# Kernel optimization log

Measured on AMD Instinct MI355X. Metric: run time of the kernel, lower is better.

## Reference

```python
import jax, jax.numpy as jnp
import numpy as np

B, S, D = 4, 4096, 2048
DECAY_BIAS_INIT = -4.0
W_SCALE = 0.02


def setup_inputs() -> dict:
    key = jax.random.key(0)
    ks = jax.random.split(key, 6)
    return {
        "x": jax.random.normal(ks[0], (B, S, D), dtype=jnp.float32),
        "W_in": jax.random.normal(ks[1], (D, D), dtype=jnp.float32) * W_SCALE,
        "b_in": jnp.zeros((D,), jnp.float32),
        "W_decay": jax.random.normal(ks[2], (D, D), dtype=jnp.float32) * W_SCALE,
        "b_decay": jnp.zeros((D,), jnp.float32),
        "W_gate": jax.random.normal(ks[3], (D, D), dtype=jnp.float32) * W_SCALE,
        "b_gate": jnp.zeros((D,), jnp.float32),
        "W_out": jax.random.normal(ks[4], (D, D), dtype=jnp.float32) * W_SCALE,
        "b_out": jnp.zeros((D,), jnp.float32),
        "decay_bias": jnp.full((D,), DECAY_BIAS_INIT, jnp.float32),
    }


def reference(x, W_in, b_in, W_decay, b_decay, W_gate, b_gate, W_out, b_out, decay_bias):
    # Projections (weights stored as [in, out]; torch Linear applies x @ W.T, here W is pre-transposed)
    inp = jax.nn.silu(jnp.einsum("bsd,de->bse", x, W_in) + b_in).astype(jnp.float32)
    decay = jax.nn.sigmoid(jnp.einsum("bsd,de->bse", x, W_decay) + b_decay + decay_bias)
    gate = jax.nn.sigmoid(jnp.einsum("bsd,de->bse", x, W_gate) + b_gate)

    # Gated linear recurrence: s_t = d_t * s_{t-1} + (1 - d_t) * i_t
    def step(state, di):
        d, i = di
        state = d * state + (1.0 - d) * i
        return state, state

    init = jnp.zeros((x.shape[0], x.shape[2]), jnp.float32)
    _, states = jax.lax.scan(
        step, init, (jnp.swapaxes(decay, 0, 1), jnp.swapaxes(inp, 0, 1))
    )  # states: [S, B, D]
    y = gate * jnp.swapaxes(states, 0, 1)  # [B, S, D]
    y = y.astype(x.dtype)
    return jnp.einsum("bsd,de->bse", y, W_out) + b_out
```

## Files before the change

### kernel.cpp

```cpp
#include <hip/hip_runtime.h>

typedef unsigned short u16;
typedef __attribute__((ext_vector_type(4))) float f4;
typedef __attribute__((ext_vector_type(8))) short s8v;
typedef __attribute__((ext_vector_type(8))) unsigned short u16x8;
typedef __attribute__((ext_vector_type(4))) unsigned short u16x4;

#define B_   4
#define S_   4096
#define D_   2048
#define M_   (B_ * S_)
#define K_   D_
#define N3_  (3 * D_)
#define CCH  128
#define LCH  32
#define NTK  32
#define SCH  8
#define SCL  16

__device__ __forceinline__ u16 f2bf(float f) {
  unsigned u = __float_as_uint(f);
  u += 0x7FFF + ((u >> 16) & 1);
  return (u16)(u >> 16);
}
__device__ __forceinline__ float bf2f(u16 h) {
  return __uint_as_float(((unsigned)h) << 16);
}
__device__ __forceinline__ float sigm(float z) {
  return 1.0f / (1.0f + __expf(-z));
}

__global__ void k_cvt(const float* __restrict__ src, u16* __restrict__ dst, int n4) {
  for (int i = blockIdx.x * 256 + threadIdx.x; i < n4; i += 2048 * 256) {
    f4 v = *(const f4*)(src + (size_t)i * 4);
    u16x4 o;
    o[0] = f2bf(v[0]); o[1] = f2bf(v[1]); o[2] = f2bf(v[2]); o[3] = f2bf(v[3]);
    *(u16x4*)(dst + (size_t)i * 4) = o;
  }
}

__global__ void k_tcvt4(const float* __restrict__ W_in, const float* __restrict__ W_dec,
                        const float* __restrict__ W_gate, const float* __restrict__ W_out,
                        u16* __restrict__ w3t, u16* __restrict__ wot) {
  __shared__ float tile[32][33];
  const float* src = (blockIdx.z == 0) ? W_in : (blockIdx.z == 1) ? W_dec
                    : (blockIdx.z == 2) ? W_gate : W_out;
  u16* dst = (blockIdx.z < 3) ? (w3t + (size_t)blockIdx.z * 2048 * 2048) : wot;
  int tx = threadIdx.x & 31, ty = threadIdx.x >> 5;
  int c0 = blockIdx.x * 32, r0 = blockIdx.y * 32;
#pragma unroll
  for (int j = 0; j < 32; j += 8)
    tile[ty + j][tx] = src[(size_t)(r0 + ty + j) * 2048 + c0 + tx];
  __syncthreads();
#pragma unroll
  for (int j = 0; j < 32; j += 8)
    dst[(size_t)(c0 + ty + j) * 2048 + r0 + tx] = f2bf(tile[tx][ty + j]);
}

__global__ void __launch_bounds__(512, 2)
k_gemm256(const u16* __restrict__ A, const u16* __restrict__ BT, int N, int mode,
          u16* __restrict__ o_inp, u16* __restrict__ o_dec, u16* __restrict__ o_gate,
          const float* __restrict__ b_in, const float* __restrict__ b_dec,
          const float* __restrict__ b_gate, const float* __restrict__ dbias,
          float* __restrict__ o_f, const float* __restrict__ b_out) {
  extern __shared__ u16 smem[];
  u16* const Asb[2] = { smem,         smem + 16384 };
  u16* const Bsb[2] = { smem + 32768, smem + 49152 };

  const int bid = blockIdx.x;
  const int xcd = bid & 7, j = bid >> 3;
  const int nsb = j >> 6;
  const int rj = j & 63;
  const int mm = rj >> 3, nn = rj & 7;
  const int tile_m = ((xcd << 3) + mm) << 8;
  const int tile_n = ((nsb << 3) + nn) << 8;

  const int tid = threadIdx.x;
  const int wave = tid >> 6, lane = tid & 63;
  const int wm = (wave >> 2) << 7;
  const int wn = (wave & 3) << 6;
  const int l15 = lane & 15, lhi = lane >> 4;
  const int srow = tid >> 3, sslot = tid & 7;

  f4 acc[8][4];
#pragma unroll
  for (int m = 0; m < 8; ++m)
#pragma unroll
    for (int n = 0; n < 4; ++n)
#pragma unroll
      for (int r = 0; r < 4; ++r) acc[m][n][r] = 0.0f;

  s8v afr2[2][2][2];
  s8v bfr[2][4];

  const int swz = l15 & 7;
  const u16* ap[2][2];
  const u16* bp[2][2];
#pragma unroll
  for (int b = 0; b < 2; ++b)
#pragma unroll
    for (int kk = 0; kk < 2; ++kk) {
      const int so = ((((kk << 2) + lhi) ^ swz) << 3);
      ap[b][kk] = Asb[b] + ((wm + l15) << 6) + so;
      bp[b][kk] = Bsb[b] + ((wn + l15) << 6) + so;
    }
  const int gl = srow * K_ + ((sslot ^ (srow & 7)) << 3);

  auto STAGE = [&](const u16* __restrict__ G, int grow0, u16* L, int c, int k0) {
    const u16* src = G + (size_t)(grow0 + (c << 6)) * K_ + k0;
    __builtin_amdgcn_global_load_lds(
        (const __attribute__((address_space(1))) unsigned int*)(src + gl),
        (__attribute__((address_space(3))) unsigned int*)(L + (((c << 6) + (wave << 3)) << 6)),
        16, 0, 0);
  };

#pragma unroll
  for (int c = 0; c < 4; ++c) STAGE(A, tile_m, Asb[0], c, 0);
#pragma unroll
  for (int c = 0; c < 4; ++c) STAGE(BT, tile_n, Bsb[0], c, 0);
#pragma unroll
  for (int c = 0; c < 4; ++c) STAGE(BT, tile_n, Bsb[1], c, 64);
  STAGE(A, tile_m, Asb[1], 0, 64);
  STAGE(A, tile_m, Asb[1], 2, 64);
  asm volatile("s_waitcnt vmcnt(6)" ::: "memory");
  __builtin_amdgcn_s_barrier();

#pragma unroll
  for (int kk = 0; kk < 2; ++kk)
#pragma unroll
    for (int mi = 0; mi < 2; ++mi)
      afr2[0][mi][kk] = *(const s8v*)(ap[0][kk] + (mi << 10));
#pragma unroll
  for (int kk = 0; kk < 2; ++kk)
#pragma unroll
    for (int n = 0; n < 4; ++n)
      bfr[kk][n] = *(const s8v*)(bp[0][kk] + (n << 10));

#pragma unroll 1
  for (int it = 0; it < NTK / 2; ++it) {
    const int t0 = it << 1;
#pragma unroll
    for (int p = 0; p < 8; ++p) {
      const int toff[8] = {1, 2, 2, 2, 2, 3, 3, 3};
      const int sopA[8] = {1, 0, 0, 1, 1, 0, 0, 1};
      const int sc0[8]  = {1, 0, 2, 0, 1, 0, 2, 0};
      const int sc1f[8] = {3, 1, 3, 2, 3, 1, 3, 2};
      const int q = p & 3;

      {
        const int st = (t0 + toff[p]) & (NTK - 1);
        const int k0s = st << 6;
        u16* const Ad = Asb[st & 1];
        u16* const Bd = Bsb[st & 1];
        if (sopA[p]) { STAGE(A, tile_m, Ad, sc0[p], k0s); STAGE(A, tile_m, Ad, sc1f[p], k0s); }
        else         { STAGE(BT, tile_n, Bd, sc0[p], k0s); STAGE(BT, tile_n, Bd, sc1f[p], k0s); }
      }
      if (q == 3) {
        asm volatile("s_waitcnt vmcnt(6)" ::: "memory");
        __builtin_amdgcn_sched_barrier(0);
      }
      __builtin_amdgcn_s_barrier();

      {
        const int pn = p + 1;
        const int qn = pn & 3, bn = (pn >> 2) & 1, as = pn & 1;
#pragma unroll
        for (int kk = 0; kk < 2; ++kk)
#pragma unroll
          for (int mi = 0; mi < 2; ++mi)
            afr2[as][mi][kk] = *(const s8v*)(ap[bn][kk] + (((qn << 1) + mi) << 10));
      }

      __builtin_amdgcn_s_setprio(1);
#pragma unroll
      for (int kk = 0; kk < 2; ++kk)
#pragma unroll
        for (int mi = 0; mi < 2; ++mi)
#pragma unroll
          for (int n = 0; n < 4; ++n)
            acc[q * 2 + mi][n] =
                __builtin_amdgcn_mfma_f32_16x16x32_bf16(afr2[p & 1][mi][kk], bfr[kk][n],
                                                        acc[q * 2 + mi][n], 0, 0, 0);
      __builtin_amdgcn_s_setprio(0);

      if (q == 3) {
        const int bn = ((p + 1) >> 2) & 1;
#pragma unroll
        for (int kk = 0; kk < 2; ++kk)
#pragma unroll
          for (int n = 0; n < 4; ++n)
            bfr[kk][n] = *(const s8v*)(bp[bn][kk] + (n << 10));
      }
    }
  }

  asm volatile("s_waitcnt vmcnt(0)" ::: "memory");
  __builtin_amdgcn_s_barrier();

  if (mode == 0) {
    const int selb = tile_n >> 11;
    const int dbase = tile_n & 2047;
    float bias[4];
#pragma unroll
    for (int n = 0; n < 4; ++n) {
      int d = dbase + wn + (n << 4) + l15;
      bias[n] = (selb == 0) ? b_in[d] : (selb == 1) ? (b_dec[d] + dbias[d]) : b_gate[d];
    }
#pragma unroll
    for (int m = 0; m < 8; ++m)
#pragma unroll
      for (int n = 0; n < 4; ++n)
#pragma unroll
        for (int r = 0; r < 4; ++r) {
          int lrow = wm + (m << 4) + (lhi << 2) + r;
          int lcol = wn + (n << 4) + l15;
          float z = acc[m][n][r] + bias[n];
          float v = (selb == 0) ? z * sigm(z) : sigm(z);
          smem[(lrow << 8) + (((lcol >> 3) ^ (lrow & 7)) << 3) + (lcol & 7)] = f2bf(v);
        }
    __builtin_amdgcn_s_barrier();
    u16* const dst = (selb == 0) ? o_inp : (selb == 1) ? o_dec : o_gate;
    const int rr = tid >> 5, sl = tid & 31;
#pragma unroll
    for (int pass = 0; pass < 16; ++pass) {
      int row = (pass << 4) + rr;
      u16x8 v = *(const u16x8*)(smem + (row << 8) + ((sl ^ (row & 7)) << 3));
      *(u16x8*)(dst + (size_t)(tile_m + row) * D_ + dbase + (sl << 3)) = v;
    }
  } else {
    float* const Tf = (float*)smem;
    f4 bo = *(const f4*)(b_out + tile_n + (lane << 2));
#pragma unroll
    for (int sw = 0; sw < 2; ++sw) {
      if (sw) __builtin_amdgcn_s_barrier();
      if ((wm >> 7) == sw) {
#pragma unroll
        for (int m = 0; m < 8; ++m)
#pragma unroll
          for (int n = 0; n < 4; ++n)
#pragma unroll
            for (int r = 0; r < 4; ++r) {
              int lrow = (m << 4) + (lhi << 2) + r;
              int lcol = wn + (n << 4) + l15;
              Tf[(lrow << 8) + (((lcol >> 2) ^ (lrow & 7)) << 2) + (lcol & 3)] = acc[m][n][r];
            }
      }
      __builtin_amdgcn_s_barrier();
#pragma unroll
      for (int pass = 0; pass < 16; ++pass) {
        int lrow = (pass << 3) + wave;
        f4 v = *(const f4*)(Tf + (lrow << 8) + ((lane ^ (lrow & 7)) << 2));
        v[0] += bo[0]; v[1] += bo[1]; v[2] += bo[2]; v[3] += bo[3];
        *(f4*)(o_f + (size_t)(tile_m + (sw << 7) + lrow) * D_ + tile_n + (lane << 2)) = v;
      }
    }
  }
}

__global__ void k_scan1(const u16* __restrict__ dec, const u16* __restrict__ inp,
                        float* __restrict__ chA, float* __restrict__ chB) {
  int b = blockIdx.x / CCH, c = blockIdx.x % CCH;
  int d0 = threadIdx.x * 8;
  const u16* dp = dec + ((size_t)b * S_ + c * LCH) * D_ + d0;
  const u16* ip = inp + ((size_t)b * S_ + c * LCH) * D_ + d0;
  float Aa[8], st[8];
#pragma unroll
  for (int i = 0; i < 8; ++i) { Aa[i] = 1.0f; st[i] = 0.0f; }
#pragma unroll 4
  for (int j = 0; j < LCH; ++j) {
    u16x8 dv = *(const u16x8*)(dp + (size_t)j * D_);
    u16x8 iv = *(const u16x8*)(ip + (size_t)j * D_);
#pragma unroll
    for (int i = 0; i < 8; ++i) {
      float dd = bf2f(dv[i]), ii = bf2f(iv[i]);
      Aa[i] *= dd;
      st[i] = dd * st[i] + (1.0f - dd) * ii;
    }
  }
  size_t o = ((size_t)b * CCH + c) * D_ + d0;
#pragma unroll
  for (int i = 0; i < 8; ++i) { chA[o + i] = Aa[i]; chB[o + i] = st[i]; }
}

__global__ void k_scan2a(const float* __restrict__ chA, const float* __restrict__ chB,
                         float* __restrict__ sA, float* __restrict__ sB) {
  int gid = blockIdx.x * 256 + threadIdx.x;
  int d = gid & (D_ - 1);
  int s = (gid >> 11) & (SCH - 1);
  int b = gid >> 14;
  float Aa = 1.0f, Bb = 0.0f;
  for (int c = 0; c < SCL; ++c) {
    size_t o = ((size_t)b * CCH + s * SCL + c) * D_ + d;
    float a = chA[o], bb = chB[o];
    Aa *= a;
    Bb = a * Bb + bb;
  }
  size_t so = ((size_t)b * SCH + s) * D_ + d;
  sA[so] = Aa; sB[so] = Bb;
}

__global__ void k_scan2b(const float* __restrict__ sA, const float* __restrict__ sB,
                         float* __restrict__ sI) {
  int gid = blockIdx.x * 256 + threadIdx.x;
  int d = gid & (D_ - 1);
  int b = gid >> 11;
  float st = 0.0f;
  for (int s = 0; s < SCH; ++s) {
    size_t o = ((size_t)b * SCH + s) * D_ + d;
    sI[o] = st;
    st = sA[o] * st + sB[o];
  }
}

__global__ void k_scan2c(const float* __restrict__ chA, const float* __restrict__ chB,
                         const float* __restrict__ sI, float* __restrict__ ini) {
  int gid = blockIdx.x * 256 + threadIdx.x;
  int d = gid & (D_ - 1);
  int s = (gid >> 11) & (SCH - 1);
  int b = gid >> 14;
  float st = sI[((size_t)b * SCH + s) * D_ + d];
  for (int c = 0; c < SCL; ++c) {
    size_t o = ((size_t)b * CCH + s * SCL + c) * D_ + d;
    ini[o] = st;
    st = chA[o] * st + chB[o];
  }
}

__global__ void k_scan3(const u16* __restrict__ dec, const u16* __restrict__ inp,
                        const u16* __restrict__ gat, const float* __restrict__ ini,
                        u16* __restrict__ y) {
  int b = blockIdx.x / CCH, c = blockIdx.x % CCH;
  int d0 = threadIdx.x * 8;
  size_t ib = ((size_t)b * CCH + c) * D_ + d0;
  float st[8];
#pragma unroll
  for (int i = 0; i < 8; ++i) st[i] = ini[ib + i];
  size_t base = ((size_t)b * S_ + c * LCH) * D_ + d0;
#pragma unroll 4
  for (int j = 0; j < LCH; ++j) {
    size_t o = base + (size_t)j * D_;
    u16x8 dv = *(const u16x8*)(dec + o);
    u16x8 iv = *(const u16x8*)(inp + o);
    u16x8 gv = *(const u16x8*)(gat + o);
    u16x8 yv;
#pragma unroll
    for (int i = 0; i < 8; ++i) {
      float dd = bf2f(dv[i]), ii = bf2f(iv[i]);
      st[i] = dd * st[i] + (1.0f - dd) * ii;
      yv[i] = f2bf(bf2f(gv[i]) * st[i]);
    }
    *(u16x8*)(y + o) = yv;
  }
}

extern "C" void kernel_launch(void* const* d_in, const int* in_sizes, int n_in,
                              void* d_out, int out_size, void* d_ws, size_t ws_size,
                              hipStream_t stream) {
  (void)in_sizes; (void)n_in; (void)out_size; (void)ws_size;
  const float* x      = (const float*)d_in[0];
  const float* W_in   = (const float*)d_in[1];
  const float* b_in   = (const float*)d_in[2];
  const float* W_dec  = (const float*)d_in[3];
  const float* b_dec  = (const float*)d_in[4];
  const float* W_gate = (const float*)d_in[5];
  const float* b_gate = (const float*)d_in[6];
  const float* W_out  = (const float*)d_in[7];
  const float* b_out  = (const float*)d_in[8];
  const float* dbias  = (const float*)d_in[9];
  float* out = (float*)d_out;

  char* ws = (char*)d_ws;
  u16*   xb  = (u16*)(ws);
  u16*   w3t = (u16*)(ws + 67108864ull);
  u16*   wot = (u16*)(ws + 92274688ull);
  u16*   inp = (u16*)(ws + 100663296ull);
  u16*   dec = (u16*)(ws + 167772160ull);
  u16*   gat = (u16*)(ws + 234881024ull);
  float* chA = (float*)(ws + 301989888ull);
  float* chB = (float*)(ws + 306184192ull);
  float* ini = (float*)(ws + 310378496ull);
  float* sA  = (float*)(ws + 314572800ull);
  float* sB  = (float*)(ws + 314834944ull);
  float* sI  = (float*)(ws + 315097088ull);
  u16*   y   = xb;

  hipFuncSetAttribute((const void*)k_gemm256,
                      hipFuncAttributeMaxDynamicSharedMemorySize, 131072);

  k_cvt<<<2048, 256, 0, stream>>>(x, xb, 8388608);
  k_tcvt4<<<dim3(64, 64, 4), 256, 0, stream>>>(W_in, W_dec, W_gate, W_out, w3t, wot);

  k_gemm256<<<(M_ / 256) * (N3_ / 256), 512, 131072, stream>>>(
      xb, w3t, N3_, 0, inp, dec, gat, b_in, b_dec, b_gate, dbias, nullptr, nullptr);

  k_scan1<<<B_ * CCH, 256, 0, stream>>>(dec, inp, chA, chB);
  k_scan2a<<<256, 256, 0, stream>>>(chA, chB, sA, sB);
  k_scan2b<<<32, 256, 0, stream>>>(sA, sB, sI);
  k_scan2c<<<256, 256, 0, stream>>>(chA, chB, sI, ini);
  k_scan3<<<B_ * CCH, 256, 0, stream>>>(dec, inp, gat, ini, y);

  k_gemm256<<<(M_ / 256) * (D_ / 256), 512, 131072, stream>>>(
      y, wot, D_, 1, nullptr, nullptr, nullptr, nullptr, nullptr, nullptr, nullptr,
      out, b_out);
}
```

Baseline: 631.8 us.

## Replace 256x256 GEMM tile with 128x256 tile, K=32 steps and higher occupancy

Rewrites the projection/output GEMM kernel to use 128x256 block tiles with K-step 32 instead of 256x256 with K-step 64. LDS use drops from 128KB to 48KB and launch bounds rise to 4 blocks per CU, trading per-block data reuse for more concurrent blocks and twice as many grid tiles. The pipeline schedule, swizzle addressing and epilogues are rewritten to match. Smaller tiles mean more global/L2 traffic per FLOP and more barriers per K-iteration.

```diff
diff --git a/kernel.cpp b/kernel.cpp
--- a/kernel.cpp
+++ b/kernel.cpp
@@ -14,9 +14,9 @@
 #define N3_  (3 * D_)
 #define CCH  128
 #define LCH  32
-#define NTK  32
 #define SCH  8
 #define SCL  16
+#define NKT  64
 
 __device__ __forceinline__ u16 f2bf(float f) {
   unsigned u = __float_as_uint(f);
@@ -57,140 +57,109 @@
     dst[(size_t)(c0 + ty + j) * 2048 + r0 + tx] = f2bf(tile[tx][ty + j]);
 }
 
-__global__ void __launch_bounds__(512, 2)
-k_gemm256(const u16* __restrict__ A, const u16* __restrict__ BT, int N, int mode,
+__global__ void __launch_bounds__(512, 4)
+k_gemm128(const u16* __restrict__ A, const u16* __restrict__ BT, int N, int mode,
           u16* __restrict__ o_inp, u16* __restrict__ o_dec, u16* __restrict__ o_gate,
           const float* __restrict__ b_in, const float* __restrict__ b_dec,
           const float* __restrict__ b_gate, const float* __restrict__ dbias,
           float* __restrict__ o_f, const float* __restrict__ b_out) {
   extern __shared__ u16 smem[];
-  u16* const Asb[2] = { smem,         smem + 16384 };
-  u16* const Bsb[2] = { smem + 32768, smem + 49152 };
+  u16* const As0 = smem;
+  u16* const As1 = smem + 4096;
+  u16* const Bs0 = smem + 8192;
+  u16* const Bs1 = smem + 16384;
 
   const int bid = blockIdx.x;
   const int xcd = bid & 7, j = bid >> 3;
-  const int nsb = j >> 6;
-  const int rj = j & 63;
-  const int mm = rj >> 3, nn = rj & 7;
-  const int tile_m = ((xcd << 3) + mm) << 8;
-  const int tile_n = ((nsb << 3) + nn) << 8;
+  const int tile_m = ((xcd << 4) + (j & 15)) << 7;
+  const int tile_n = (j >> 4) << 8;
 
   const int tid = threadIdx.x;
   const int wave = tid >> 6, lane = tid & 63;
-  const int wm = (wave >> 2) << 7;
+  const int wm = (wave >> 2) << 6;
   const int wn = (wave & 3) << 6;
   const int l15 = lane & 15, lhi = lane >> 4;
-  const int srow = tid >> 3, sslot = tid & 7;
-
-  f4 acc[8][4];
-#pragma unroll
-  for (int m = 0; m < 8; ++m)
+
+  const int slog = (tid & 7) ^ ((tid >> 3) & 7);
+  const int gl = ((((tid >> 3) << 1) + (slog >> 2)) * K_) + ((slog & 3) << 3);
+  const int ldst = (wave << 9);
+
+  const int phys = (((l15 & 1) << 2) + lhi) ^ ((l15 >> 1) & 7);
+  const int rbase = ((l15 >> 1) << 6) + (phys << 3);
+  const u16* const apb[2] = { As0 + (wm << 5) + rbase, As1 + (wm << 5) + rbase };
+  const u16* const bpb[2] = { Bs0 + (wn << 5) + rbase, Bs1 + (wn << 5) + rbase };
+
+  f4 acc[4][4];
+#pragma unroll
+  for (int m = 0; m < 4; ++m)
 #pragma unroll
     for (int n = 0; n < 4; ++n)
 #pragma unroll
       for (int r = 0; r < 4; ++r) acc[m][n][r] = 0.0f;
 
-  s8v afr2[2][2][2];
-  s8v bfr[2][4];
-
-  const int swz = l15 & 7;
-  const u16* ap[2][2];
-  const u16* bp[2][2];
-#pragma unroll
-  for (int b = 0; b < 2; ++b)
-#pragma unroll
-    for (int kk = 0; kk < 2; ++kk) {
-      const int so = ((((kk << 2) + lhi) ^ swz) << 3);
-      ap[b][kk] = Asb[b] + ((wm + l15) << 6) + so;
-      bp[b][kk] = Bsb[b] + ((wn + l15) << 6) + so;
-    }
-  const int gl = srow * K_ + ((sslot ^ (srow & 7)) << 3);
+  s8v afr2[2][2];
+  s8v bfr[4];
 
   auto STAGE = [&](const u16* __restrict__ G, int grow0, u16* L, int c, int k0) {
-    const u16* src = G + (size_t)(grow0 + (c << 6)) * K_ + k0;
+    const u16* src = G + (size_t)(grow0 + (c << 7)) * K_ + k0;
     __builtin_amdgcn_global_load_lds(
         (const __attribute__((address_space(1))) unsigned int*)(src + gl),
-        (__attribute__((address_space(3))) unsigned int*)(L + (((c << 6) + (wave << 3)) << 6)),
+        (__attribute__((address_space(3))) unsigned int*)(L + (c << 12) + ldst),
         16, 0, 0);
   };
 
-#pragma unroll
-  for (int c = 0; c < 4; ++c) STAGE(A, tile_m, Asb[0], c, 0);
-#pragma unroll
-  for (int c = 0; c < 4; ++c) STAGE(BT, tile_n, Bsb[0], c, 0);
-#pragma unroll
-  for (int c = 0; c < 4; ++c) STAGE(BT, tile_n, Bsb[1], c, 64);
-  STAGE(A, tile_m, Asb[1], 0, 64);
-  STAGE(A, tile_m, Asb[1], 2, 64);
-  asm volatile("s_waitcnt vmcnt(6)" ::: "memory");
+  STAGE(A, tile_m, As0, 0, 0);
+  STAGE(BT, tile_n, Bs0, 0, 0); STAGE(BT, tile_n, Bs0, 1, 0);
+  STAGE(A, tile_m, As1, 0, 32);
+  STAGE(BT, tile_n, Bs1, 0, 32); STAGE(BT, tile_n, Bs1, 1, 32);
+  asm volatile("s_waitcnt vmcnt(3)" ::: "memory");
   __builtin_amdgcn_s_barrier();
-
-#pragma unroll
-  for (int kk = 0; kk < 2; ++kk)
-#pragma unroll
-    for (int mi = 0; mi < 2; ++mi)
-      afr2[0][mi][kk] = *(const s8v*)(ap[0][kk] + (mi << 10));
-#pragma unroll
-  for (int kk = 0; kk < 2; ++kk)
-#pragma unroll
-    for (int n = 0; n < 4; ++n)
-      bfr[kk][n] = *(const s8v*)(bp[0][kk] + (n << 10));
+#pragma unroll
+  for (int i = 0; i < 2; ++i) afr2[0][i] = *(const s8v*)(apb[0] + i * 512);
+#pragma unroll
+  for (int nf = 0; nf < 4; ++nf) bfr[nf] = *(const s8v*)(bpb[0] + nf * 512);
 
 #pragma unroll 1
-  for (int it = 0; it < NTK / 2; ++it) {
-    const int t0 = it << 1;
-#pragma unroll
-    for (int p = 0; p < 8; ++p) {
-      const int toff[8] = {1, 2, 2, 2, 2, 3, 3, 3};
-      const int sopA[8] = {1, 0, 0, 1, 1, 0, 0, 1};
-      const int sc0[8]  = {1, 0, 2, 0, 1, 0, 2, 0};
-      const int sc1f[8] = {3, 1, 3, 2, 3, 1, 3, 2};
-      const int q = p & 3;
+  for (int it = 0; it < NKT / 2; ++it) {
+    const int t = it << 1;
+#pragma unroll
+    for (int half = 0; half < 2; ++half) {
+      const int tt = t + half;
+      const int cur = half, nxt = half ^ 1;
+      u16* const Acur = half ? As1 : As0;  (void)Acur;
+      u16* const Anxt = half ? As0 : As1;
+      u16* const Bcur = half ? Bs1 : Bs0;
+
+      STAGE(A, tile_m, Anxt, 0, ((tt + 1) & (NKT - 1)) << 5);
+      __builtin_amdgcn_s_barrier();
+#pragma unroll
+      for (int i = 0; i < 2; ++i) afr2[1][i] = *(const s8v*)(apb[cur] + (2 + i) * 512);
+      __builtin_amdgcn_s_setprio(1);
+#pragma unroll
+      for (int i = 0; i < 2; ++i)
+#pragma unroll
+        for (int nf = 0; nf < 4; ++nf)
+          acc[i][nf] = __builtin_amdgcn_mfma_f32_16x16x32_bf16(afr2[0][i], bfr[nf], acc[i][nf], 0, 0, 0);
+      __builtin_amdgcn_s_setprio(0);
 
       {
-        const int st = (t0 + toff[p]) & (NTK - 1);
-        const int k0s = st << 6;
-        u16* const Ad = Asb[st & 1];
-        u16* const Bd = Bsb[st & 1];
-        if (sopA[p]) { STAGE(A, tile_m, Ad, sc0[p], k0s); STAGE(A, tile_m, Ad, sc1f[p], k0s); }
-        else         { STAGE(BT, tile_n, Bd, sc0[p], k0s); STAGE(BT, tile_n, Bd, sc1f[p], k0s); }
-      }
-      if (q == 3) {
-        asm volatile("s_waitcnt vmcnt(6)" ::: "memory");
-        __builtin_amdgcn_sched_barrier(0);
-      }
-      __builtin_amdgcn_s_barrier();
-
-      {
-        const int pn = p + 1;
-        const int qn = pn & 3, bn = (pn >> 2) & 1, as = pn & 1;
-#pragma unroll
-        for (int kk = 0; kk < 2; ++kk)
-#pragma unroll
-          for (int mi = 0; mi < 2; ++mi)
-            afr2[as][mi][kk] = *(const s8v*)(ap[bn][kk] + (((qn << 1) + mi) << 10));
-      }
-
+        const int k2 = ((tt + 2) & (NKT - 1)) << 5;
+        STAGE(BT, tile_n, Bcur, 0, k2); STAGE(BT, tile_n, Bcur, 1, k2);
+      }
+      asm volatile("s_waitcnt vmcnt(2)" ::: "memory");
+      __builtin_amdgcn_sched_barrier(0);
+      __builtin_amdgcn_s_barrier();
+#pragma unroll
+      for (int i = 0; i < 2; ++i) afr2[0][i] = *(const s8v*)(apb[nxt] + i * 512);
       __builtin_amdgcn_s_setprio(1);
 #pragma unroll
-      for (int kk = 0; kk < 2; ++kk)
-#pragma unroll
-        for (int mi = 0; mi < 2; ++mi)
-#pragma unroll
-          for (int n = 0; n < 4; ++n)
-            acc[q * 2 + mi][n] =
-                __builtin_amdgcn_mfma_f32_16x16x32_bf16(afr2[p & 1][mi][kk], bfr[kk][n],
-                                                        acc[q * 2 + mi][n], 0, 0, 0);
+      for (int i = 0; i < 2; ++i)
+#pragma unroll
+        for (int nf = 0; nf < 4; ++nf)
+          acc[2 + i][nf] = __builtin_amdgcn_mfma_f32_16x16x32_bf16(afr2[1][i], bfr[nf], acc[2 + i][nf], 0, 0, 0);
       __builtin_amdgcn_s_setprio(0);
-
-      if (q == 3) {
-        const int bn = ((p + 1) >> 2) & 1;
-#pragma unroll
-        for (int kk = 0; kk < 2; ++kk)
-#pragma unroll
-          for (int n = 0; n < 4; ++n)
-            bfr[kk][n] = *(const s8v*)(bp[bn][kk] + (n << 10));
-      }
+#pragma unroll
+      for (int nf = 0; nf < 4; ++nf) bfr[nf] = *(const s8v*)(bpb[nxt] + nf * 512);
     }
   }
 
@@ -200,59 +169,70 @@
   if (mode == 0) {
     const int selb = tile_n >> 11;
     const int dbase = tile_n & 2047;
+    u16* const dst = (selb == 0) ? o_inp : (selb == 1) ? o_dec : o_gate;
     float bias[4];
 #pragma unroll
-    for (int n = 0; n < 4; ++n) {
-      int d = dbase + wn + (n << 4) + l15;
-      bias[n] = (selb == 0) ? b_in[d] : (selb == 1) ? (b_dec[d] + dbias[d]) : b_gate[d];
-    }
-#pragma unroll
-    for (int m = 0; m < 8; ++m)
-#pragma unroll
-      for (int n = 0; n < 4; ++n)
-#pragma unroll
-        for (int r = 0; r < 4; ++r) {
-          int lrow = wm + (m << 4) + (lhi << 2) + r;
-          int lcol = wn + (n << 4) + l15;
-          float z = acc[m][n][r] + bias[n];
-          float v = (selb == 0) ? z * sigm(z) : sigm(z);
-          smem[(lrow << 8) + (((lcol >> 3) ^ (lrow & 7)) << 3) + (lcol & 7)] = f2bf(v);
-        }
-    __builtin_amdgcn_s_barrier();
-    u16* const dst = (selb == 0) ? o_inp : (selb == 1) ? o_dec : o_gate;
+    for (int nf = 0; nf < 4; ++nf) {
+      int d = dbase + wn + (nf << 4) + l15;
+      bias[nf] = (selb == 0) ? b_in[d] : (selb == 1) ? (b_dec[d] + dbias[d]) : b_gate[d];
+    }
     const int rr = tid >> 5, sl = tid & 31;
 #pragma unroll
-    for (int pass = 0; pass < 16; ++pass) {
-      int row = (pass << 4) + rr;
-      u16x8 v = *(const u16x8*)(smem + (row << 8) + ((sl ^ (row & 7)) << 3));
-      *(u16x8*)(dst + (size_t)(tile_m + row) * D_ + dbase + (sl << 3)) = v;
+    for (int sw = 0; sw < 2; ++sw) {
+      if ((wm >> 6) == sw) {
+#pragma unroll
+        for (int mf = 0; mf < 4; ++mf)
+#pragma unroll
+          for (int nf = 0; nf < 4; ++nf)
+#pragma unroll
+            for (int r = 0; r < 4; ++r) {
+              int lrow = (mf << 4) + (lhi << 2) + r;
+              int lcol = wn + (nf << 4) + l15;
+              float z = acc[mf][nf][r] + bias[nf];
+              float v = (selb == 0) ? z * sigm(z) : sigm(z);
+              smem[(lrow << 8) + (((lcol >> 3) ^ (lrow & 7)) << 3) + (lcol & 7)] = f2bf(v);
+            }
+      }
+      asm volatile("s_waitcnt lgkmcnt(0)" ::: "memory");
+      __builtin_amdgcn_s_barrier();
+#pragma unroll
+      for (int pass = 0; pass < 4; ++pass) {
+        int row = (pass << 4) + rr;
+        u16x8 v = *(const u16x8*)(smem + (row << 8) + ((sl ^ (row & 7)) << 3));
+        *(u16x8*)(dst + (size_t)(tile_m + (sw << 6) + row) * D_ + dbase + (sl << 3)) = v;
+      }
+      asm volatile("s_waitcnt lgkmcnt(0)" ::: "memory");
+      __builtin_amdgcn_s_barrier();
     }
   } else {
     float* const Tf = (float*)smem;
     f4 bo = *(const f4*)(b_out + tile_n + (lane << 2));
 #pragma unroll
-    for (int sw = 0; sw < 2; ++sw) {
-      if (sw) __builtin_amdgcn_s_barrier();
-      if ((wm >> 7) == sw) {
-#pragma unroll
-        for (int m = 0; m < 8; ++m)
-#pragma unroll
-          for (int n = 0; n < 4; ++n)
+    for (int sw = 0; sw < 4; ++sw) {
+      if ((wm >> 6) == (sw >> 1)) {
+        const int mb = (sw & 1) << 1;
+#pragma unroll
+        for (int mm = 0; mm < 2; ++mm)
+#pragma unroll
+          for (int nf = 0; nf < 4; ++nf)
 #pragma unroll
             for (int r = 0; r < 4; ++r) {
-              int lrow = (m << 4) + (lhi << 2) + r;
-              int lcol = wn + (n << 4) + l15;
-              Tf[(lrow << 8) + (((lcol >> 2) ^ (lrow & 7)) << 2) + (lcol & 3)] = acc[m][n][r];
+              int lrow = (mm << 4) + (lhi << 2) + r;
+              int lcol = wn + (nf << 4) + l15;
+              Tf[(lrow << 8) + (((lcol >> 2) ^ (lrow & 7)) << 2) + (lcol & 3)] = acc[mb + mm][nf][r];
             }
       }
-      __builtin_amdgcn_s_barrier();
-#pragma unroll
-      for (int pass = 0; pass < 16; ++pass) {
+      asm volatile("s_waitcnt lgkmcnt(0)" ::: "memory");
+      __builtin_amdgcn_s_barrier();
+#pragma unroll
+      for (int pass = 0; pass < 4; ++pass) {
         int lrow = (pass << 3) + wave;
         f4 v = *(const f4*)(Tf + (lrow << 8) + ((lane ^ (lrow & 7)) << 2));
         v[0] += bo[0]; v[1] += bo[1]; v[2] += bo[2]; v[3] += bo[3];
-        *(f4*)(o_f + (size_t)(tile_m + (sw << 7) + lrow) * D_ + tile_n + (lane << 2)) = v;
-      }
+        *(f4*)(o_f + (size_t)(tile_m + (sw << 5) + lrow) * D_ + tile_n + (lane << 2)) = v;
+      }
+      asm volatile("s_waitcnt lgkmcnt(0)" ::: "memory");
+      __builtin_amdgcn_s_barrier();
     }
   }
 }
@@ -384,13 +364,13 @@
   float* sI  = (float*)(ws + 315097088ull);
   u16*   y   = xb;
 
-  hipFuncSetAttribute((const void*)k_gemm256,
-                      hipFuncAttributeMaxDynamicSharedMemorySize, 131072);
+  hipFuncSetAttribute((const void*)k_gemm128,
+                      hipFuncAttributeMaxDynamicSharedMemorySize, 49152);
 
   k_cvt<<<2048, 256, 0, stream>>>(x, xb, 8388608);
   k_tcvt4<<<dim3(64, 64, 4), 256, 0, stream>>>(W_in, W_dec, W_gate, W_out, w3t, wot);
 
-  k_gemm256<<<(M_ / 256) * (N3_ / 256), 512, 131072, stream>>>(
+  k_gemm128<<<(M_ / 128) * (N3_ / 256), 512, 49152, stream>>>(
       xb, w3t, N3_, 0, inp, dec, gat, b_in, b_dec, b_gate, dbias, nullptr, nullptr);
 
   k_scan1<<<B_ * CCH, 256, 0, stream>>>(dec, inp, chA, chB);
@@ -399,7 +379,7 @@
   k_scan2c<<<256, 256, 0, stream>>>(chA, chB, sI, ini);
   k_scan3<<<B_ * CCH, 256, 0, stream>>>(dec, inp, gat, ini, y);
 
-  k_gemm256<<<(M_ / 256) * (D_ / 256), 512, 131072, stream>>>(
+  k_gemm128<<<(M_ / 128) * (D_ / 256), 512, 49152, stream>>>(
       y, wot, D_, 1, nullptr, nullptr, nullptr, nullptr, nullptr, nullptr, nullptr,
       out, b_out);
 }
```

Result: slower. 722.5 us (+14.4%).
